# Performance work log

Measured on AMD Instinct MI355X. Metric: run time of the kernel, lower is better.

The kernel has to match this reference:

```python
import jax, jax.numpy as jnp
import numpy as np

EPS = 1e-9

def dice(x, alpha):
    # Dice: batch-norm over dim 0 (unbiased var, ddof=1), then gated blend.
    mu = jnp.mean(x, axis=0)
    var = jnp.var(x, axis=0, ddof=1)
    p = jax.nn.sigmoid((x - mu) / jnp.sqrt(var + EPS))
    return alpha * x * (1.0 - p) + x * p


def setup_inputs() -> dict:
    key = jax.random.key(0)
    ks = jax.random.split(key, 8)
    bs, seq, dim = 2048, 200, 64
    d_in = dim * 4
    return {
        "query": jax.random.normal(ks[0], (bs, dim), jnp.float32),
        "user_behavior": jax.random.normal(ks[1], (bs, seq, dim), jnp.float32),
        "mask": jax.random.uniform(ks[2], (bs, seq, 1), jnp.float32),
        "W1": jax.random.normal(ks[3], (d_in, 32), jnp.float32) / np.sqrt(d_in),
        "b1": jnp.zeros((32,), jnp.float32),
        "alpha1": jnp.zeros((1,), jnp.float32),
        "W2": jax.random.normal(ks[4], (32, 16), jnp.float32) / np.sqrt(32.0),
        "b2": jnp.zeros((16,), jnp.float32),
        "alpha2": jnp.zeros((1,), jnp.float32),
        "W3": jax.random.normal(ks[5], (16, 1), jnp.float32) / np.sqrt(16.0),
        "b3": jnp.zeros((1,), jnp.float32),
    }


def reference(query, user_behavior, mask, W1, b1, alpha1, W2, b2, alpha2, W3, b3):
    # query: (bs, dim) -> broadcast to (bs, seq, dim)
    q = jnp.broadcast_to(query[:, None, :], user_behavior.shape)
    attn_input = jnp.concatenate(
        [q, user_behavior, q - user_behavior, q * user_behavior], axis=-1
    )  # (bs, seq, 4*dim)
    h = dice(attn_input @ W1 + b1, alpha1)
    h = dice(h @ W2 + b2, alpha2)
    attns = h @ W3 + b3  # (bs, seq, 1)
    attns = attns * mask
    output = jnp.sum(user_behavior * attns, axis=1)  # (bs, dim)
    return output, attns
```

## Files before the change

kernel.cpp:

```cpp
#include <hip/hip_runtime.h>
#include <math.h>

#define BS  2048
#define SEQ 200
#define DIM 64
#define C1  32
#define C2  16

typedef __attribute__((ext_vector_type(8))) short bf16x8_t;
typedef __attribute__((ext_vector_type(4))) float f32x4_t;

__device__ __forceinline__ float dice1(float x, float m, float r, float al) {
    float t = (x - m) * r;
    float p = 1.f / (1.f + __expf(-t));
    return x * (al + p * (1.f - al));
}

__device__ __forceinline__ unsigned short f2bf(float f) {
    union { float f; unsigned u; } a;
    a.f = f;
    unsigned r = a.u + 0x7fff + ((a.u >> 16) & 1);
    return (unsigned short)(r >> 16);
}

__device__ __forceinline__ float bf2f(short h) {
    union { unsigned u; float f; } a;
    a.u = ((unsigned)(unsigned short)h) << 16;
    return a.f;
}

__global__ __launch_bounds__(256) void k_gemm1(const float* __restrict__ q,
                                               const float* __restrict__ ub,
                                               const float* __restrict__ W1,
                                               const float* __restrict__ b1,
                                               short* __restrict__ z1) {
    const int bs = blockIdx.x;
    const int tid = threadIdx.x;
    __shared__ __align__(16) short s_B[2 * 2 * 64 * 8];
    __shared__ __align__(16) float s_qw[C1];
    __shared__ __align__(16) short s_z[208 * C1];

    const float* qrow = q + bs * DIM;

    {
        const int kt = tid >> 7;
        const int nt = (tid >> 6) & 1;
        const int l  = tid & 63;
        const int c  = nt * 16 + (l & 15);
        bf16x8_t bfr;
        #pragma unroll
        for (int j = 0; j < 8; ++j) {
            int k = kt * 32 + ((l >> 4) << 3) + j;
            float wb = W1[(64 + k) * C1 + c] - W1[(128 + k) * C1 + c]
                     + qrow[k] * W1[(192 + k) * C1 + c];
            bfr[j] = (short)f2bf(wb);
        }
        *(bf16x8_t*)((char*)s_B + (((kt * 2 + nt) * 64) + l) * 16) = bfr;
    }
    if (tid < C1) {
        float a = b1[tid];
        #pragma unroll 8
        for (int d = 0; d < DIM; ++d)
            a = fmaf(qrow[d], W1[d * C1 + tid] + W1[(128 + d) * C1 + tid], a);
        s_qw[tid] = a;
    }
    __syncthreads();

    const int wave = tid >> 6;
    const int l = tid & 63;
    const int g = l >> 4;
    const bf16x8_t b00 = *(const bf16x8_t*)((char*)s_B + (0 * 64 + l) * 16);
    const bf16x8_t b01 = *(const bf16x8_t*)((char*)s_B + (1 * 64 + l) * 16);
    const bf16x8_t b10 = *(const bf16x8_t*)((char*)s_B + (2 * 64 + l) * 16);
    const bf16x8_t b11 = *(const bf16x8_t*)((char*)s_B + (3 * 64 + l) * 16);
    const float qw0 = s_qw[l & 15];
    const float qw1 = s_qw[16 + (l & 15)];
    const float* ubb = ub + (size_t)bs * SEQ * DIM;

    for (int mt = wave; mt < 13; mt += 4) {
        int row = mt * 16 + (l & 15);
        int rc = row > SEQ - 1 ? SEQ - 1 : row;
        const float* rp = ubb + rc * DIM + g * 8;
        float4 f0 = *(const float4*)(rp);
        float4 f1 = *(const float4*)(rp + 4);
        float4 f2 = *(const float4*)(rp + 32);
        float4 f3 = *(const float4*)(rp + 36);
        bf16x8_t a0, a1;
        a0[0] = (short)f2bf(f0.x); a0[1] = (short)f2bf(f0.y);
        a0[2] = (short)f2bf(f0.z); a0[3] = (short)f2bf(f0.w);
        a0[4] = (short)f2bf(f1.x); a0[5] = (short)f2bf(f1.y);
        a0[6] = (short)f2bf(f1.z); a0[7] = (short)f2bf(f1.w);
        a1[0] = (short)f2bf(f2.x); a1[1] = (short)f2bf(f2.y);
        a1[2] = (short)f2bf(f2.z); a1[3] = (short)f2bf(f2.w);
        a1[4] = (short)f2bf(f3.x); a1[5] = (short)f2bf(f3.y);
        a1[6] = (short)f2bf(f3.z); a1[7] = (short)f2bf(f3.w);
        f32x4_t acc0 = {0.f, 0.f, 0.f, 0.f};
        f32x4_t acc1 = {0.f, 0.f, 0.f, 0.f};
        acc0 = __builtin_amdgcn_mfma_f32_16x16x32_bf16(a0, b00, acc0, 0, 0, 0);
        acc0 = __builtin_amdgcn_mfma_f32_16x16x32_bf16(a1, b10, acc0, 0, 0, 0);
        acc1 = __builtin_amdgcn_mfma_f32_16x16x32_bf16(a0, b01, acc1, 0, 0, 0);
        acc1 = __builtin_amdgcn_mfma_f32_16x16x32_bf16(a1, b11, acc1, 0, 0, 0);
        const int orow = mt * 16 + g * 4;
        #pragma unroll
        for (int r = 0; r < 4; ++r) {
            s_z[(orow + r) * C1 + (l & 15)]      = (short)f2bf(acc0[r] + qw0);
            s_z[(orow + r) * C1 + 16 + (l & 15)] = (short)f2bf(acc1[r] + qw1);
        }
    }
    __syncthreads();
    bf16x8_t* dst = (bf16x8_t*)(z1 + (size_t)bs * SEQ * C1);
    const bf16x8_t* srcl = (const bf16x8_t*)s_z;
    for (int i = tid; i < SEQ * C1 / 8; i += 256) dst[i] = srcl[i];
}

__global__ __launch_bounds__(256) void k_redA1(const short* __restrict__ z1,
                                               float* __restrict__ pS,
                                               float* __restrict__ pQ) {
    const int seq = blockIdx.x;
    const int part = blockIdx.y;
    const int tid = threadIdx.x;
    const int cq = tid & 3;
    float s[8], qq[8];
    #pragma unroll
    for (int j = 0; j < 8; ++j) { s[j] = 0.f; qq[j] = 0.f; }
    #pragma unroll
    for (int it = 0; it < 4; ++it) {
        int b = part * 256 + (tid >> 2) + it * 64;
        bf16x8_t v = *(const bf16x8_t*)(z1 + ((size_t)b * SEQ + seq) * C1 + cq * 8);
        #pragma unroll
        for (int j = 0; j < 8; ++j) {
            float f = bf2f(v[j]);
            s[j] += f;
            qq[j] = fmaf(f, f, qq[j]);
        }
    }
    #pragma unroll
    for (int st = 4; st <= 32; st <<= 1) {
        #pragma unroll
        for (int j = 0; j < 8; ++j) {
            s[j]  += __shfl_xor(s[j],  st);
            qq[j] += __shfl_xor(qq[j], st);
        }
    }
    __shared__ float shS[4][4][8], shQ[4][4][8];
    const int wave = tid >> 6, l = tid & 63;
    if (l < 4) {
        #pragma unroll
        for (int j = 0; j < 8; ++j) { shS[wave][l][j] = s[j]; shQ[wave][l][j] = qq[j]; }
    }
    __syncthreads();
    if (tid < 32) {
        int c4 = tid >> 3, j = tid & 7;
        float a = shS[0][c4][j] + shS[1][c4][j] + shS[2][c4][j] + shS[3][c4][j];
        float b = shQ[0][c4][j] + shQ[1][c4][j] + shQ[2][c4][j] + shQ[3][c4][j];
        pS[((size_t)part * SEQ + seq) * C1 + c4 * 8 + j] = a;
        pQ[((size_t)part * SEQ + seq) * C1 + c4 * 8 + j] = b;
    }
}

__global__ __launch_bounds__(256) void k_gemm2s(const short* __restrict__ z1,
                                                const float* __restrict__ pS1,
                                                const float* __restrict__ pQ1,
                                                const float* __restrict__ alpha1,
                                                const float* __restrict__ W2,
                                                const float* __restrict__ b2,
                                                short* __restrict__ z2,
                                                float* __restrict__ pS2,
                                                float* __restrict__ pQ2) {
    const int strip = blockIdx.x;
    const int part = blockIdx.y;
    const int tid = threadIdx.x;
    __shared__ float s_mu[8][C1];
    __shared__ float s_rs[8][C1];

    {
        int ss = tid >> 5, c = tid & 31;
        int seqg = strip * 8 + ss;
        float s = 0.f, q = 0.f;
        #pragma unroll
        for (int p = 0; p < 8; ++p) {
            s += pS1[((size_t)p * SEQ + seqg) * C1 + c];
            q += pQ1[((size_t)p * SEQ + seqg) * C1 + c];
        }
        float m = s / (float)BS;
        float var = (q - s * m) / (float)(BS - 1);
        s_mu[ss][c] = m;
        s_rs[ss][c] = rsqrtf(var + 1e-9f);
    }
    const int wave = tid >> 6;
    const int l = tid & 63;
    const int g = l >> 4;
    const int cB = l & 15;
    bf16x8_t bw;
    #pragma unroll
    for (int j = 0; j < 8; ++j) bw[j] = (short)f2bf(W2[(g * 8 + j) * C2 + cB]);
    const float bias = b2[cB];
    const float al = alpha1[0];
    __syncthreads();

    const int cb = (l & 3) * 8;
    const int srcLane = (l & 15) * 4 + g;
    for (int sq = wave * 2; sq < wave * 2 + 2; ++sq) {
        const int seqg = strip * 8 + sq;
        float sumS = 0.f, sumQ = 0.f;
        for (int t = 0; t < 16; ++t) {
            const int b0 = part * 256 + t * 16;
            const int brow = b0 + (l >> 2);
            bf16x8_t zv = *(const bf16x8_t*)(z1 + ((size_t)brow * SEQ + seqg) * C1 + cb);
            union { bf16x8_t v; int w[4]; } hp;
            #pragma unroll
            for (int j = 0; j < 8; ++j) {
                float x = bf2f(zv[j]);
                hp.v[j] = (short)f2bf(dice1(x, s_mu[sq][cb + j], s_rs[sq][cb + j], al));
            }
            union { bf16x8_t v; int w[4]; } af;
            #pragma unroll
            for (int w4 = 0; w4 < 4; ++w4) af.w[w4] = __shfl(hp.w[w4], srcLane);
            f32x4_t acc = {bias, bias, bias, bias};
            acc = __builtin_amdgcn_mfma_f32_16x16x32_bf16(af.v, bw, acc, 0, 0, 0);
            #pragma unroll
            for (int r = 0; r < 4; ++r) {
                int rb = b0 + g * 4 + r;
                z2[((size_t)rb * SEQ + seqg) * C2 + cB] = (short)f2bf(acc[r]);
                sumS += acc[r];
                sumQ = fmaf(acc[r], acc[r], sumQ);
            }
        }
        sumS += __shfl_xor(sumS, 16); sumS += __shfl_xor(sumS, 32);
        sumQ += __shfl_xor(sumQ, 16); sumQ += __shfl_xor(sumQ, 32);
        if (l < 16) {
            pS2[((size_t)part * SEQ + seqg) * C2 + cB] = sumS;
            pQ2[((size_t)part * SEQ + seqg) * C2 + cB] = sumQ;
        }
    }
}

__global__ __launch_bounds__(64) void k_redB2(const float* __restrict__ pS,
                                              const float* __restrict__ pQ,
                                              float* __restrict__ mu,
                                              float* __restrict__ rstd) {
    const int cell = blockIdx.x * 64 + threadIdx.x;
    const int seq = cell >> 4, c = cell & 15;
    float s = 0.f, q = 0.f;
    #pragma unroll
    for (int p = 0; p < 8; ++p) {
        s += pS[((size_t)p * SEQ + seq) * C2 + c];
        q += pQ[((size_t)p * SEQ + seq) * C2 + c];
    }
    float m = s / (float)BS;
    float var = (q - s * m) / (float)(BS - 1);
    mu[seq * C2 + c] = m;
    rstd[seq * C2 + c] = rsqrtf(var + 1e-9f);
}

__global__ __launch_bounds__(256) void k_final(const short* __restrict__ z2,
                                               const float* __restrict__ mu2,
                                               const float* __restrict__ rstd2,
                                               const float* __restrict__ alpha2,
                                               const float* __restrict__ W3,
                                               const float* __restrict__ b3,
                                               const float* __restrict__ mask,
                                               const float* __restrict__ ub,
                                               float* __restrict__ out,
                                               float* __restrict__ attns) {
    const int bs = blockIdx.x;
    const int tid = threadIdx.x;
    __shared__ float s_attn[SEQ];
    __shared__ float s_w3[C2];
    __shared__ __align__(16) float4 s_pool[256];
    if (tid < C2) s_w3[tid] = W3[tid];
    __syncthreads();
    if (tid < SEQ) {
        const float al = alpha2[0];
        const float bb3 = b3[0];
        bf16x8_t v0 = *(const bf16x8_t*)(z2 + ((size_t)bs * SEQ + tid) * C2);
        bf16x8_t v1 = *(const bf16x8_t*)(z2 + ((size_t)bs * SEQ + tid) * C2 + 8);
        const float4* m4 = (const float4*)(mu2 + tid * C2);
        const float4* r4 = (const float4*)(rstd2 + tid * C2);
        float a = bb3;
        #pragma unroll
        for (int k = 0; k < 4; ++k) {
            float4 m = m4[k], r = r4[k];
            float x0 = bf2f(k < 2 ? v0[k * 4 + 0] : v1[(k - 2) * 4 + 0]);
            float x1 = bf2f(k < 2 ? v0[k * 4 + 1] : v1[(k - 2) * 4 + 1]);
            float x2 = bf2f(k < 2 ? v0[k * 4 + 2] : v1[(k - 2) * 4 + 2]);
            float x3 = bf2f(k < 2 ? v0[k * 4 + 3] : v1[(k - 2) * 4 + 3]);
            a = fmaf(dice1(x0, m.x, r.x, al), s_w3[k * 4 + 0], a);
            a = fmaf(dice1(x1, m.y, r.y, al), s_w3[k * 4 + 1], a);
            a = fmaf(dice1(x2, m.z, r.z, al), s_w3[k * 4 + 2], a);
            a = fmaf(dice1(x3, m.w, r.w, al), s_w3[k * 4 + 3], a);
        }
        a *= mask[bs * SEQ + tid];
        s_attn[tid] = a;
        attns[(size_t)bs * SEQ + tid] = a;
    }
    __syncthreads();
    const int dq = tid & 15;
    const int sg = tid >> 4;
    float4 acc = {0.f, 0.f, 0.f, 0.f};
    const float4* ub4 = (const float4*)(ub + (size_t)bs * SEQ * DIM);
    for (int s = sg; s < SEQ; s += 16) {
        float a = s_attn[s];
        float4 v = ub4[s * 16 + dq];
        acc.x = fmaf(v.x, a, acc.x);
        acc.y = fmaf(v.y, a, acc.y);
        acc.z = fmaf(v.z, a, acc.z);
        acc.w = fmaf(v.w, a, acc.w);
    }
    s_pool[tid] = acc;
    for (int h = 8; h > 0; h >>= 1) {
        __syncthreads();
        if (sg < h) {
            float4 o = s_pool[tid + h * 16];
            acc.x += o.x; acc.y += o.y; acc.z += o.z; acc.w += o.w;
            s_pool[tid] = acc;
        }
    }
    if (sg == 0)
        *(float4*)(out + (size_t)bs * DIM + dq * 4) = acc;
}

extern "C" void kernel_launch(void* const* d_in, const int* in_sizes, int n_in,
                              void* d_out, int out_size, void* d_ws, size_t ws_size,
                              hipStream_t stream) {
    const float* q    = (const float*)d_in[0];
    const float* ub   = (const float*)d_in[1];
    const float* mask = (const float*)d_in[2];
    const float* W1   = (const float*)d_in[3];
    const float* b1   = (const float*)d_in[4];
    const float* a1   = (const float*)d_in[5];
    const float* W2   = (const float*)d_in[6];
    const float* b2   = (const float*)d_in[7];
    const float* a2   = (const float*)d_in[8];
    const float* W3   = (const float*)d_in[9];
    const float* b3   = (const float*)d_in[10];

    float* out   = (float*)d_out;
    float* attns = out + (size_t)BS * DIM;

    float* ws = (float*)d_ws;
    short* z1 = (short*)ws;
    short* z2 = z1 + (size_t)BS * SEQ * C1;
    float* fw = (float*)(z2 + (size_t)BS * SEQ * C2);
    float* pS1 = fw;
    float* pQ1 = pS1 + 8 * SEQ * C1;
    float* pS2 = pQ1 + 8 * SEQ * C1;
    float* pQ2 = pS2 + 8 * SEQ * C2;
    float* mu2   = pQ2 + 8 * SEQ * C2;
    float* rstd2 = mu2 + SEQ * C2;

    hipLaunchKernelGGL(k_gemm1, dim3(BS), dim3(256), 0, stream, q, ub, W1, b1, z1);
    hipLaunchKernelGGL(k_redA1, dim3(SEQ, 8), dim3(256), 0, stream, z1, pS1, pQ1);
    hipLaunchKernelGGL(k_gemm2s, dim3(25, 8), dim3(256), 0, stream,
                       z1, pS1, pQ1, a1, W2, b2, z2, pS2, pQ2);
    hipLaunchKernelGGL(k_redB2, dim3(50), dim3(64), 0, stream, pS2, pQ2, mu2, rstd2);
    hipLaunchKernelGGL(k_final, dim3(BS), dim3(256), 0, stream,
                       z2, mu2, rstd2, a2, W3, b3, mask, ub, out, attns);
}
```

Before: 249.8 us.

## Fuse batch-norm reductions into MLP kernels and use atomics for layer-2 stats

Removes the separate layer-1 and layer-2 statistic reduction kernels. The layer-2 GEMM kernel now computes the full layer-1 mean/variance itself for its seq strip, by scanning all batch rows. Layer-2 partial sums are accumulated with atomics into a zeroed buffer, and every final block recomputes mu/rstd into LDS. This saves kernel launches and intermediate buffers, but each part-block redundantly rereads all of z1 for its strip. It also makes every final block redo the per-cell normalization math.

```diff
diff --git a/kernel.cpp b/kernel.cpp
--- a/kernel.cpp
+++ b/kernel.cpp
@@ -113,82 +113,66 @@
     for (int i = tid; i < SEQ * C1 / 8; i += 256) dst[i] = srcl[i];
 }
 
-__global__ __launch_bounds__(256) void k_redA1(const short* __restrict__ z1,
-                                               float* __restrict__ pS,
-                                               float* __restrict__ pQ) {
-    const int seq = blockIdx.x;
-    const int part = blockIdx.y;
-    const int tid = threadIdx.x;
-    const int cq = tid & 3;
-    float s[8], qq[8];
-    #pragma unroll
-    for (int j = 0; j < 8; ++j) { s[j] = 0.f; qq[j] = 0.f; }
-    #pragma unroll
-    for (int it = 0; it < 4; ++it) {
-        int b = part * 256 + (tid >> 2) + it * 64;
-        bf16x8_t v = *(const bf16x8_t*)(z1 + ((size_t)b * SEQ + seq) * C1 + cq * 8);
-        #pragma unroll
-        for (int j = 0; j < 8; ++j) {
-            float f = bf2f(v[j]);
-            s[j] += f;
-            qq[j] = fmaf(f, f, qq[j]);
-        }
-    }
-    #pragma unroll
-    for (int st = 4; st <= 32; st <<= 1) {
-        #pragma unroll
-        for (int j = 0; j < 8; ++j) {
-            s[j]  += __shfl_xor(s[j],  st);
-            qq[j] += __shfl_xor(qq[j], st);
-        }
-    }
-    __shared__ float shS[4][4][8], shQ[4][4][8];
-    const int wave = tid >> 6, l = tid & 63;
-    if (l < 4) {
-        #pragma unroll
-        for (int j = 0; j < 8; ++j) { shS[wave][l][j] = s[j]; shQ[wave][l][j] = qq[j]; }
-    }
-    __syncthreads();
-    if (tid < 32) {
-        int c4 = tid >> 3, j = tid & 7;
-        float a = shS[0][c4][j] + shS[1][c4][j] + shS[2][c4][j] + shS[3][c4][j];
-        float b = shQ[0][c4][j] + shQ[1][c4][j] + shQ[2][c4][j] + shQ[3][c4][j];
-        pS[((size_t)part * SEQ + seq) * C1 + c4 * 8 + j] = a;
-        pQ[((size_t)part * SEQ + seq) * C1 + c4 * 8 + j] = b;
-    }
-}
-
-__global__ __launch_bounds__(256) void k_gemm2s(const short* __restrict__ z1,
-                                                const float* __restrict__ pS1,
-                                                const float* __restrict__ pQ1,
-                                                const float* __restrict__ alpha1,
-                                                const float* __restrict__ W2,
-                                                const float* __restrict__ b2,
-                                                short* __restrict__ z2,
-                                                float* __restrict__ pS2,
-                                                float* __restrict__ pQ2) {
+__global__ __launch_bounds__(256) void k_mlp2(const short* __restrict__ z1,
+                                              const float* __restrict__ alpha1,
+                                              const float* __restrict__ W2,
+                                              const float* __restrict__ b2,
+                                              short* __restrict__ z2,
+                                              float* __restrict__ aS2,
+                                              float* __restrict__ aQ2) {
     const int strip = blockIdx.x;
     const int part = blockIdx.y;
     const int tid = threadIdx.x;
+    const int wave = tid >> 6;
+    const int l = tid & 63;
     __shared__ float s_mu[8][C1];
     __shared__ float s_rs[8][C1];
+    __shared__ float redS[4][4][8], redQ[4][4][8];
 
     {
-        int ss = tid >> 5, c = tid & 31;
-        int seqg = strip * 8 + ss;
-        float s = 0.f, q = 0.f;
-        #pragma unroll
-        for (int p = 0; p < 8; ++p) {
-            s += pS1[((size_t)p * SEQ + seqg) * C1 + c];
-            q += pQ1[((size_t)p * SEQ + seqg) * C1 + c];
-        }
-        float m = s / (float)BS;
-        float var = (q - s * m) / (float)(BS - 1);
-        s_mu[ss][c] = m;
-        s_rs[ss][c] = rsqrtf(var + 1e-9f);
-    }
-    const int wave = tid >> 6;
-    const int l = tid & 63;
+        const int cq = tid & 3;
+        const int rg = tid >> 2;
+        for (int ss = 0; ss < 8; ++ss) {
+            const int seqg = strip * 8 + ss;
+            float s[8], qq[8];
+            #pragma unroll
+            for (int j = 0; j < 8; ++j) { s[j] = 0.f; qq[j] = 0.f; }
+            for (int it = 0; it < BS / 64; ++it) {
+                int b = rg + it * 64;
+                bf16x8_t v = *(const bf16x8_t*)(z1 + ((size_t)b * SEQ + seqg) * C1 + cq * 8);
+                #pragma unroll
+                for (int j = 0; j < 8; ++j) {
+                    float f = bf2f(v[j]);
+                    s[j] += f;
+                    qq[j] = fmaf(f, f, qq[j]);
+                }
+            }
+            #pragma unroll
+            for (int st = 4; st <= 32; st <<= 1) {
+                #pragma unroll
+                for (int j = 0; j < 8; ++j) {
+                    s[j]  += __shfl_xor(s[j],  st);
+                    qq[j] += __shfl_xor(qq[j], st);
+                }
+            }
+            if (l < 4) {
+                #pragma unroll
+                for (int j = 0; j < 8; ++j) { redS[wave][l][j] = s[j]; redQ[wave][l][j] = qq[j]; }
+            }
+            __syncthreads();
+            if (tid < 32) {
+                int c4 = tid >> 3, j = tid & 7;
+                float a = redS[0][c4][j] + redS[1][c4][j] + redS[2][c4][j] + redS[3][c4][j];
+                float b = redQ[0][c4][j] + redQ[1][c4][j] + redQ[2][c4][j] + redQ[3][c4][j];
+                float m = a / (float)BS;
+                float var = (b - a * m) / (float)(BS - 1);
+                s_mu[ss][c4 * 8 + j] = m;
+                s_rs[ss][c4 * 8 + j] = rsqrtf(var + 1e-9f);
+            }
+            __syncthreads();
+        }
+    }
+
     const int g = l >> 4;
     const int cB = l & 15;
     bf16x8_t bw;
@@ -196,7 +180,6 @@
     for (int j = 0; j < 8; ++j) bw[j] = (short)f2bf(W2[(g * 8 + j) * C2 + cB]);
     const float bias = b2[cB];
     const float al = alpha1[0];
-    __syncthreads();
 
     const int cb = (l & 3) * 8;
     const int srcLane = (l & 15) * 4 + g;
@@ -229,33 +212,15 @@
         sumS += __shfl_xor(sumS, 16); sumS += __shfl_xor(sumS, 32);
         sumQ += __shfl_xor(sumQ, 16); sumQ += __shfl_xor(sumQ, 32);
         if (l < 16) {
-            pS2[((size_t)part * SEQ + seqg) * C2 + cB] = sumS;
-            pQ2[((size_t)part * SEQ + seqg) * C2 + cB] = sumQ;
-        }
-    }
-}
-
-__global__ __launch_bounds__(64) void k_redB2(const float* __restrict__ pS,
-                                              const float* __restrict__ pQ,
-                                              float* __restrict__ mu,
-                                              float* __restrict__ rstd) {
-    const int cell = blockIdx.x * 64 + threadIdx.x;
-    const int seq = cell >> 4, c = cell & 15;
-    float s = 0.f, q = 0.f;
-    #pragma unroll
-    for (int p = 0; p < 8; ++p) {
-        s += pS[((size_t)p * SEQ + seq) * C2 + c];
-        q += pQ[((size_t)p * SEQ + seq) * C2 + c];
-    }
-    float m = s / (float)BS;
-    float var = (q - s * m) / (float)(BS - 1);
-    mu[seq * C2 + c] = m;
-    rstd[seq * C2 + c] = rsqrtf(var + 1e-9f);
+            atomicAdd(&aS2[seqg * C2 + cB], sumS);
+            atomicAdd(&aQ2[seqg * C2 + cB], sumQ);
+        }
+    }
 }
 
 __global__ __launch_bounds__(256) void k_final(const short* __restrict__ z2,
-                                               const float* __restrict__ mu2,
-                                               const float* __restrict__ rstd2,
+                                               const float* __restrict__ aS2,
+                                               const float* __restrict__ aQ2,
                                                const float* __restrict__ alpha2,
                                                const float* __restrict__ W3,
                                                const float* __restrict__ b3,
@@ -265,30 +230,31 @@
                                                float* __restrict__ attns) {
     const int bs = blockIdx.x;
     const int tid = threadIdx.x;
+    __shared__ float lmu[SEQ * 17];
+    __shared__ float lrs[SEQ * 17];
     __shared__ float s_attn[SEQ];
     __shared__ float s_w3[C2];
     __shared__ __align__(16) float4 s_pool[256];
     if (tid < C2) s_w3[tid] = W3[tid];
+    for (int cell = tid; cell < SEQ * C2; cell += 256) {
+        int seq = cell >> 4, c = cell & 15;
+        float s = aS2[cell], qv = aQ2[cell];
+        float m = s / (float)BS;
+        float var = (qv - s * m) / (float)(BS - 1);
+        lmu[seq * 17 + c] = m;
+        lrs[seq * 17 + c] = rsqrtf(var + 1e-9f);
+    }
     __syncthreads();
     if (tid < SEQ) {
         const float al = alpha2[0];
         const float bb3 = b3[0];
         bf16x8_t v0 = *(const bf16x8_t*)(z2 + ((size_t)bs * SEQ + tid) * C2);
         bf16x8_t v1 = *(const bf16x8_t*)(z2 + ((size_t)bs * SEQ + tid) * C2 + 8);
-        const float4* m4 = (const float4*)(mu2 + tid * C2);
-        const float4* r4 = (const float4*)(rstd2 + tid * C2);
         float a = bb3;
         #pragma unroll
-        for (int k = 0; k < 4; ++k) {
-            float4 m = m4[k], r = r4[k];
-            float x0 = bf2f(k < 2 ? v0[k * 4 + 0] : v1[(k - 2) * 4 + 0]);
-            float x1 = bf2f(k < 2 ? v0[k * 4 + 1] : v1[(k - 2) * 4 + 1]);
-            float x2 = bf2f(k < 2 ? v0[k * 4 + 2] : v1[(k - 2) * 4 + 2]);
-            float x3 = bf2f(k < 2 ? v0[k * 4 + 3] : v1[(k - 2) * 4 + 3]);
-            a = fmaf(dice1(x0, m.x, r.x, al), s_w3[k * 4 + 0], a);
-            a = fmaf(dice1(x1, m.y, r.y, al), s_w3[k * 4 + 1], a);
-            a = fmaf(dice1(x2, m.z, r.z, al), s_w3[k * 4 + 2], a);
-            a = fmaf(dice1(x3, m.w, r.w, al), s_w3[k * 4 + 3], a);
+        for (int c = 0; c < C2; ++c) {
+            float x = bf2f(c < 8 ? v0[c] : v1[c - 8]);
+            a = fmaf(dice1(x, lmu[tid * 17 + c], lrs[tid * 17 + c], al), s_w3[c], a);
         }
         a *= mask[bs * SEQ + tid];
         s_attn[tid] = a;
@@ -341,19 +307,13 @@
     float* ws = (float*)d_ws;
     short* z1 = (short*)ws;
     short* z2 = z1 + (size_t)BS * SEQ * C1;
-    float* fw = (float*)(z2 + (size_t)BS * SEQ * C2);
-    float* pS1 = fw;
-    float* pQ1 = pS1 + 8 * SEQ * C1;
-    float* pS2 = pQ1 + 8 * SEQ * C1;
-    float* pQ2 = pS2 + 8 * SEQ * C2;
-    float* mu2   = pQ2 + 8 * SEQ * C2;
-    float* rstd2 = mu2 + SEQ * C2;
-
+    float* aS2 = (float*)(z2 + (size_t)BS * SEQ * C2);
+    float* aQ2 = aS2 + SEQ * C2;
+
+    hipMemsetAsync(aS2, 0, (size_t)SEQ * C2 * 2 * sizeof(float), stream);
     hipLaunchKernelGGL(k_gemm1, dim3(BS), dim3(256), 0, stream, q, ub, W1, b1, z1);
-    hipLaunchKernelGGL(k_redA1, dim3(SEQ, 8), dim3(256), 0, stream, z1, pS1, pQ1);
-    hipLaunchKernelGGL(k_gemm2s, dim3(25, 8), dim3(256), 0, stream,
-                       z1, pS1, pQ1, a1, W2, b2, z2, pS2, pQ2);
-    hipLaunchKernelGGL(k_redB2, dim3(50), dim3(64), 0, stream, pS2, pQ2, mu2, rstd2);
+    hipLaunchKernelGGL(k_mlp2, dim3(25, 8), dim3(256), 0, stream,
+                       z1, a1, W2, b2, z2, aS2, aQ2);
     hipLaunchKernelGGL(k_final, dim3(BS), dim3(256), 0, stream,
-                       z2, mu2, rstd2, a2, W3, b3, mask, ub, out, attns);
-}
+                       z2, aS2, aQ2, a2, W3, b3, mask, ub, out, attns);
+}
```

New measurement: 300.5 us. 20.3% more time.
